# Kernel tuning notes

Hardware: AMD Instinct MI355X
Metric: run time of the kernel (lower is better)

The kernel has to match this reference:

```python
import jax, jax.numpy as jnp
import numpy as np

BETA = 1.0  # inverse temperature (default of retrieve())
EPS = 1e-12  # matches torch F.normalize eps


def _l2_normalize(x):
    # torch.nn.functional.normalize(p=2, dim=-1): x / max(||x||, eps)
    n = jnp.sqrt(jnp.sum(x * x, axis=-1, keepdims=True))
    return x / jnp.maximum(n, EPS)


def setup_inputs() -> dict:
    key = jax.random.key(0)
    kq, kk = jax.random.split(key)
    N, K, D = 65536, 4096, 128
    queries = jax.random.normal(kq, (N, D), dtype=jnp.float32)
    # learnable memory keys, init_std = 0.02
    keys = jax.random.normal(kk, (K, D), dtype=jnp.float32) * 0.02
    return {"queries": queries, "keys": keys}


def reference(queries, keys):
    # normalize_keys=True, normalize_queries=True
    k_n = _l2_normalize(keys)
    q_n = _l2_normalize(queries)
    # values are TIED to the raw keys parameter (get_values returns self.keys,
    # un-normalized) — only the score-side keys are normalized.
    values = keys
    scores = BETA * jnp.einsum('nd,kd->nk', q_n, k_n)  # [N, K]
    attention = jax.nn.softmax(scores, axis=-1)
    retrieved = jnp.einsum('nk,kd->nd', attention, values)  # [N, D]
    return retrieved
```

## Files before the change

### kernel.cpp

```cpp
#include <hip/hip_runtime.h>
#include <hip/hip_bf16.h>
#include <stdint.h>


typedef __attribute__((ext_vector_type(8))) short bf16x8;
typedef __attribute__((ext_vector_type(16))) float f32x16;

#define MFMA32(a, b, c) __builtin_amdgcn_mfma_f32_32x32x16_bf16(a, b, c, 0, 0, 0)
#define ASYNC_CP16(gsrc, ldst)                                                  \
  __builtin_amdgcn_global_load_lds(                                             \
      (const __attribute__((address_space(1))) void*)(gsrc),                    \
      (__attribute__((address_space(3))) void*)(ldst), 16, 0, 0)

__device__ __forceinline__ unsigned pkbf(float lo, float hi) {
  union { __hip_bfloat162 h2; unsigned u; } v;
  v.h2 = __float22bfloat162_rn(float2{lo, hi});
  return v.u;
}

__global__ __launch_bounds__(256) void prep_k(const float* __restrict__ k,
                                              char* __restrict__ knf,
                                              char* __restrict__ vtf, int K) {
  __shared__ float sRaw[64 * 132];
  __shared__ float sScale[64];
  const int tid = threadIdx.x;
  const int kbase = blockIdx.x * 64;
  {
    const int key_loc = tid >> 2, dq = tid & 3;
    const float4* src = (const float4*)(k + (size_t)(kbase + key_loc) * 128 + dq * 32);
    float4 f[8];
    float ss = 0.f;
#pragma unroll
    for (int i = 0; i < 8; ++i) {
      f[i] = src[i];
      ss += f[i].x * f[i].x + f[i].y * f[i].y + f[i].z * f[i].z + f[i].w * f[i].w;
    }
    ss += __shfl_xor(ss, 1);
    ss += __shfl_xor(ss, 2);
    float4* dst = (float4*)(sRaw + key_loc * 132 + dq * 32);
#pragma unroll
    for (int i = 0; i < 8; ++i) dst[i] = f[i];
    if (dq == 0) sScale[key_loc] = ss > 0.f ? rsqrtf(ss) : 0.f;
  }
  __syncthreads();

#pragma unroll
  for (int r = 0; r < 4; ++r) {
    const int c = r * 256 + tid;
    const int t_loc = c >> 9, ds = (c >> 6) & 7, l = c & 63;
    const int h5 = l >> 5, c32 = l & 31;
    const int key_loc = t_loc * 32 + c32;
    const float sc = sScale[key_loc];
    const float* p = sRaw + key_loc * 132 + ds * 16 + h5 * 8;
    uint4 w;
    w.x = pkbf(p[0] * sc, p[1] * sc);
    w.y = pkbf(p[2] * sc, p[3] * sc);
    w.z = pkbf(p[4] * sc, p[5] * sc);
    w.w = pkbf(p[6] * sc, p[7] * sc);
    *(uint4*)(knf + ((size_t)blockIdx.x * 1024 + c) * 16) = w;
  }
#pragma unroll
  for (int r = 0; r < 4; ++r) {
    const int c = r * 256 + tid;
    const int s = c >> 8, db2 = (c >> 6) & 3, l = c & 63;
    const int h5 = l >> 5, c32 = l & 31;
    const int d = db2 * 32 + c32;
    const int kb = (s >> 1) * 32 + (s & 1) * 8 + h5 * 4;
    float f[8];
#pragma unroll
    for (int j = 0; j < 8; ++j)
      f[j] = sRaw[(kb + (j & 3) + (j >> 2) * 16) * 132 + d];
    uint4 w;
    w.x = pkbf(f[0], f[1]);
    w.y = pkbf(f[2], f[3]);
    w.z = pkbf(f[4], f[5]);
    w.w = pkbf(f[6], f[7]);
    *(uint4*)(vtf + ((size_t)blockIdx.x * 1024 + c) * 16) = w;
  }
}

__global__ __launch_bounds__(256, 2) void attn_main(
    const float* __restrict__ q, const char* __restrict__ knf,
    const char* __restrict__ vtf, float* __restrict__ out, int K) {
  __shared__ __align__(16) char sK[2][16384];
  const int tid = threadIdx.x;
  const int wave = tid >> 6, lane = tid & 63;
  const int h5 = lane >> 5, c32 = lane & 31;
  const int qrow0 = blockIdx.x * 128 + wave * 32;

  bf16x8 qf[8];
  {
    const float* qr = q + (size_t)(qrow0 + c32) * 128;
    float f[64];
    float ss = 0.f;
#pragma unroll
    for (int ds = 0; ds < 8; ++ds) {
      const float4 a = *(const float4*)(qr + ds * 16 + h5 * 8);
      const float4 b = *(const float4*)(qr + ds * 16 + h5 * 8 + 4);
      f[ds * 8 + 0] = a.x; f[ds * 8 + 1] = a.y; f[ds * 8 + 2] = a.z; f[ds * 8 + 3] = a.w;
      f[ds * 8 + 4] = b.x; f[ds * 8 + 5] = b.y; f[ds * 8 + 6] = b.z; f[ds * 8 + 7] = b.w;
    }
#pragma unroll
    for (int i = 0; i < 64; ++i) ss += f[i] * f[i];
    ss += __shfl_xor(ss, 32);
    const float sc = (ss > 0.f ? rsqrtf(ss) : 0.f) * 1.44269504f;
#pragma unroll
    for (int ds = 0; ds < 8; ++ds) {
      union { unsigned u[4]; bf16x8 v; } t;
#pragma unroll
      for (int p = 0; p < 4; ++p)
        t.u[p] = pkbf(f[ds * 8 + 2 * p] * sc, f[ds * 8 + 2 * p + 1] * sc);
      qf[ds] = t.v;
    }
  }

  f32x16 acc[4];
#pragma unroll
  for (int db2 = 0; db2 < 4; ++db2)
#pragma unroll
    for (int r = 0; r < 16; ++r) acc[db2][r] = 0.f;
  float den = 0.f;
  f32x16 Zf;
#pragma unroll
  for (int r = 0; r < 16; ++r) Zf[r] = 0.f;

  union pfu { unsigned u[4]; bf16x8 v; };
  pfu pf[4];

  const int nIter = K >> 6;
  auto stage = [&](int it, int buf) {
#pragma unroll
    for (int i = 0; i < 4; ++i)
      ASYNC_CP16(knf + (size_t)it * 16384 + (wave * 4 + i) * 1024 + lane * 16,
                 sK[buf] + (wave * 4 + i) * 1024);
  };

  auto computeS = [&](int buf, f32x16* S) {
#pragma unroll
    for (int t = 0; t < 2; ++t) {
      f32x16 s;
#pragma unroll
      for (int ds = 0; ds < 8; ++ds) {
        const bf16x8 kf = *(const bf16x8*)(sK[buf] + (t * 8 + ds) * 1024 + lane * 16);
        s = MFMA32(kf, qf[ds], (ds == 0) ? Zf : s);
      }
      S[t] = s;
    }
  };

  auto doPV = [&](int m) {
    const char* vbase = vtf + (size_t)m * 16384;
    bf16x8 vcur[4], vnxt[4];
#pragma unroll
    for (int db2 = 0; db2 < 4; ++db2)
      vcur[db2] = *(const bf16x8*)(vbase + db2 * 1024 + lane * 16);
#pragma unroll
    for (int s = 0; s < 4; ++s) {
      if (s < 3)
#pragma unroll
        for (int db2 = 0; db2 < 4; ++db2)
          vnxt[db2] = *(const bf16x8*)(vbase + ((s + 1) * 4 + db2) * 1024 + lane * 16);
#pragma unroll
      for (int db2 = 0; db2 < 4; ++db2)
        acc[db2] = MFMA32(vcur[db2], pf[s].v, acc[db2]);
      if (s < 3)
#pragma unroll
        for (int db2 = 0; db2 < 4; ++db2) vcur[db2] = vnxt[db2];
    }
  };

  auto doExp = [&](const f32x16* S) {
#pragma unroll
    for (int s = 0; s < 4; ++s) {
      const int t = s >> 1, w = s & 1;
      float e[8];
#pragma unroll
      for (int j = 0; j < 8; ++j) {
        const int rr = w * 4 + (j & 3) + (j >> 2) * 8;
        e[j] = __builtin_amdgcn_exp2f(S[t][rr]);
      }
      den += ((e[0] + e[1]) + (e[2] + e[3])) + ((e[4] + e[5]) + (e[6] + e[7]));
#pragma unroll
      for (int j2 = 0; j2 < 4; ++j2) pf[s].u[j2] = pkbf(e[2 * j2], e[2 * j2 + 1]);
    }
  };

  stage(0, 0);
  __syncthreads();
  stage(1, 1);
  {
    f32x16 S[2];
    computeS(0, S);
    doExp(S);
  }
  for (int it = 1; it < nIter; ++it) {
    const int buf = it & 1;
    __syncthreads();
    if (it + 1 < nIter) stage(it + 1, buf ^ 1);
    f32x16 S[2];
    computeS(buf, S);
    doPV(it - 1);
    doExp(S);
  }
  doPV(nIter - 1);

  den += __shfl_xor(den, 32);
  const float rd = 1.0f / den;

  __syncthreads();
  float* wls = (float*)(&sK[0][0] + wave * 4096);
#pragma unroll
  for (int db2 = 0; db2 < 4; ++db2) {
#pragma unroll
    for (int qd = 0; qd < 4; ++qd) {
      float4 v;
      v.x = acc[db2][qd * 4 + 0] * rd;
      v.y = acc[db2][qd * 4 + 1] * rd;
      v.z = acc[db2][qd * 4 + 2] * rd;
      v.w = acc[db2][qd * 4 + 3] * rd;
      *(float4*)(wls + c32 * 32 + (((h5 + 2 * qd) ^ (c32 & 7)) << 2)) = v;
    }
#pragma unroll
    for (int p = 0; p < 4; ++p) {
      const int ql = p * 8 + (lane >> 3);
      const int x = lane & 7;
      const float4 v = *(const float4*)(wls + ql * 32 + ((x ^ (ql & 7)) << 2));
      *(float4*)(out + (size_t)(qrow0 + ql) * 128 + db2 * 32 + x * 4) = v;
    }
  }
}

extern "C" void kernel_launch(void* const* d_in, const int* in_sizes, int n_in,
                              void* d_out, int out_size, void* d_ws, size_t ws_size,
                              hipStream_t stream) {
  const float* q = (const float*)d_in[0];
  const float* k = (const float*)d_in[1];
  const int N = in_sizes[0] / 128;
  const int K = in_sizes[1] / 128;
  char* ws = (char*)d_ws;
  char* knf = ws;
  char* vtf = ws + (size_t)K * 256;
  float* out = (float*)d_out;

  prep_k<<<dim3(K / 64), dim3(256), 0, stream>>>(k, knf, vtf, K);
  attn_main<<<dim3(N / 128), dim3(256), 0, stream>>>(q, knf, vtf, out, K);
}
```

Measured before the change: 221.9 us.

## Software-pipeline QK and exp across iterations with ping-pong score buffers and setprio

Restructures the main loop so the QK^T scores for tile i+1 are computed before exp and PV of tile i, using two score register sets and a loop unrolled by two. The first V fragments are loaded early, and MFMA sections are wrapped in s_setprio to favour this wave's compute. The goal is to hide exp latency and global V-load latency behind MFMA work. The cost is extra live registers (another two f32x16 score tiles), which may push against the 2-blocks-per-CU occupancy limit or cause spills.

```diff
diff --git a/kernel.cpp b/kernel.cpp
--- a/kernel.cpp
+++ b/kernel.cpp
@@ -126,8 +126,11 @@
 
   union pfu { unsigned u[4]; bf16x8 v; };
   pfu pf[4];
+  f32x16 Sa[2], Sb[2];
+  bf16x8 vcur[4];
 
   const int nIter = K >> 6;
+
   auto stage = [&](int it, int buf) {
 #pragma unroll
     for (int i = 0; i < 4; ++i)
@@ -148,27 +151,6 @@
     }
   };
 
-  auto doPV = [&](int m) {
-    const char* vbase = vtf + (size_t)m * 16384;
-    bf16x8 vcur[4], vnxt[4];
-#pragma unroll
-    for (int db2 = 0; db2 < 4; ++db2)
-      vcur[db2] = *(const bf16x8*)(vbase + db2 * 1024 + lane * 16);
-#pragma unroll
-    for (int s = 0; s < 4; ++s) {
-      if (s < 3)
-#pragma unroll
-        for (int db2 = 0; db2 < 4; ++db2)
-          vnxt[db2] = *(const bf16x8*)(vbase + ((s + 1) * 4 + db2) * 1024 + lane * 16);
-#pragma unroll
-      for (int db2 = 0; db2 < 4; ++db2)
-        acc[db2] = MFMA32(vcur[db2], pf[s].v, acc[db2]);
-      if (s < 3)
-#pragma unroll
-        for (int db2 = 0; db2 < 4; ++db2) vcur[db2] = vnxt[db2];
-    }
-  };
-
   auto doExp = [&](const f32x16* S) {
 #pragma unroll
     for (int s = 0; s < 4; ++s) {
@@ -185,23 +167,67 @@
     }
   };
 
+  auto loadV0 = [&](int m) {
+    const char* vbase = vtf + (size_t)m * 16384;
+#pragma unroll
+    for (int db2 = 0; db2 < 4; ++db2)
+      vcur[db2] = *(const bf16x8*)(vbase + db2 * 1024 + lane * 16);
+  };
+
+  auto doPV = [&](int m) {
+    const char* vbase = vtf + (size_t)m * 16384;
+    bf16x8 vnxt[4];
+#pragma unroll
+    for (int s = 0; s < 4; ++s) {
+      if (s < 3)
+#pragma unroll
+        for (int db2 = 0; db2 < 4; ++db2)
+          vnxt[db2] = *(const bf16x8*)(vbase + ((s + 1) * 4 + db2) * 1024 + lane * 16);
+#pragma unroll
+      for (int db2 = 0; db2 < 4; ++db2)
+        acc[db2] = MFMA32(vcur[db2], pf[s].v, acc[db2]);
+      if (s < 3)
+#pragma unroll
+        for (int db2 = 0; db2 < 4; ++db2) vcur[db2] = vnxt[db2];
+    }
+  };
+
   stage(0, 0);
   __syncthreads();
   stage(1, 1);
-  {
-    f32x16 S[2];
-    computeS(0, S);
-    doExp(S);
-  }
-  for (int it = 1; it < nIter; ++it) {
-    const int buf = it & 1;
+  computeS(0, Sa);
+
+  __syncthreads();
+  stage(2, 0);
+  loadV0(0);
+  __builtin_amdgcn_s_setprio(1);
+  computeS(1, Sb);
+  doExp(Sa);
+  doPV(0);
+  __builtin_amdgcn_s_setprio(0);
+
+  for (int itp = 2; itp < nIter; itp += 2) {
     __syncthreads();
-    if (it + 1 < nIter) stage(it + 1, buf ^ 1);
-    f32x16 S[2];
-    computeS(buf, S);
-    doPV(it - 1);
-    doExp(S);
-  }
+    stage(itp + 1, 1);
+    loadV0(itp - 1);
+    __builtin_amdgcn_s_setprio(1);
+    computeS(0, Sa);
+    doExp(Sb);
+    doPV(itp - 1);
+    __builtin_amdgcn_s_setprio(0);
+
+    __syncthreads();
+    if (itp + 2 < nIter) stage(itp + 2, 0);
+    loadV0(itp);
+    __builtin_amdgcn_s_setprio(1);
+    computeS(1, Sb);
+    doExp(Sa);
+    doPV(itp);
+    __builtin_amdgcn_s_setprio(0);
+  }
+
+  loadV0(nIter - 1);
+  doExp(Sb);
   doPV(nIter - 1);
 
   den += __shfl_xor(den, 32);
```

Measured after the change: 218.5 us. About the same (-1.6%).
